# Optimization experiments

Hardware: AMD Instinct MI355X
Metric: run time of the kernel (lower is better)

Reference implementation:

```python
import jax, jax.numpy as jnp
import numpy as np

N, D, H, N_HEADS = 2048, 512, 512, 16

def setup_inputs() -> dict:
    key = jax.random.key(0)
    k1, k2, k3 = jax.random.split(key, 3)
    inputs = jax.random.normal(k1, (N, D), dtype=jnp.float32)
    idx = jax.random.randint(k2, (N,), 0, N_HEADS, dtype=jnp.int64)
    weights = jax.random.normal(k3, (N_HEADS, D, H), dtype=jnp.float32)
    biases = jnp.zeros((N_HEADS, H), dtype=jnp.float32)
    return {"inputs": inputs, "idx": idx, "weights": weights, "biases": biases}

def reference(inputs, idx, weights, biases):
    # per-sample weight gather: (N, D, H) then batched vec-mat: (N, 1, D) @ (N, D, H) -> (N, H)
    w = weights[idx]            # (N, D, H)  -- the redundant materialized gather
    b = biases[idx]             # (N, H)
    return jnp.einsum('nd,ndh->nh', inputs, w) + b
```

## Files before the change

### kernel.cpp

```cpp
#include <hip/hip_runtime.h>


#define N_SAMPLES 2048
#define DIM       512
#define HDIM      512
#define N_HEADS   16
#define SH        32
#define BPITCH    520

typedef __attribute__((ext_vector_type(8))) short bf16x8;
typedef __attribute__((ext_vector_type(4))) float floatx4;

__device__ inline unsigned short f2bf_rne(float f) {
    union { float f; unsigned u; } v; v.f = f;
    return (unsigned short)((v.u + 0x7FFFu + ((v.u >> 16) & 1u)) >> 16);
}
__device__ inline unsigned bfpack_rne(float lo, float hi) {
    return (unsigned)f2bf_rne(lo) | ((unsigned)f2bf_rne(hi) << 16);
}

__global__ __launch_bounds__(512, 2) void fused(
    const float* __restrict__ x,
    const int*   __restrict__ idx,
    const float* __restrict__ w,
    const float* __restrict__ bias,
    float*       __restrict__ out)
{
    __shared__ unsigned short Bl[SH * BPITCH];
    __shared__ unsigned short slist[N_SAMPLES];
    __shared__ int wcnt[8];

    const int bid  = blockIdx.x;
    const int head = 2 * (bid & 7) + ((bid >> 3) & 1);
    const int h0   = (bid >> 4) * SH;
    const int t    = threadIdx.x;
    const int wave = t >> 6;
    const int lane = t & 63;
    const int l16  = lane & 15;
    const int quad = lane >> 4;

    int myidx[4];
    #pragma unroll
    for (int c = 0; c < 4; ++c)
        myidx[c] = idx[(wave * 4 + c) * 64 + lane];

    const int hh = (t & 7) * 4;
    const int dg = t >> 3;
    const float* wg = w + (size_t)head * DIM * HDIM + h0;
    float4 q[8];
    #pragma unroll
    for (int s = 0; s < 8; ++s)
        q[s] = *(const float4*)(wg + (size_t)(dg * 8 + s) * HDIM + hh);

    unsigned long long masks[4];
    {
        int mycnt = 0;
        #pragma unroll
        for (int c = 0; c < 4; ++c) {
            masks[c] = __ballot(myidx[c] == head);
            mycnt += __popcll(masks[c]);
        }
        if (lane == 0) wcnt[wave] = mycnt;
    }
    __syncthreads();
    int cnt = 0, base = 0;
    #pragma unroll
    for (int i = 0; i < 8; ++i) { if (i < wave) base += wcnt[i]; cnt += wcnt[i]; }
    {
        int pos = base;
        #pragma unroll
        for (int c = 0; c < 4; ++c) {
            const unsigned long long m = masks[c];
            if (m & (1ull << lane)) {
                const int rank = __popcll(m & ((1ull << lane) - 1ull));
                slist[pos + rank] = (unsigned short)((wave * 4 + c) * 64 + lane);
            }
            pos += __popcll(m);
        }
    }

    #pragma unroll
    for (int k = 0; k < 4; ++k) {
        uint4 o;
        o.x = bfpack_rne(((const float*)&q[0])[k], ((const float*)&q[1])[k]);
        o.y = bfpack_rne(((const float*)&q[2])[k], ((const float*)&q[3])[k]);
        o.z = bfpack_rne(((const float*)&q[4])[k], ((const float*)&q[5])[k]);
        o.w = bfpack_rne(((const float*)&q[6])[k], ((const float*)&q[7])[k]);
        *(uint4*)&Bl[(hh + k) * BPITCH + dg * 8] = o;
    }
    __syncthreads();

    const int   mt  = (cnt + 15) >> 4;
    const float bv0 = bias[head * HDIM + h0 + l16];
    const float bv1 = bias[head * HDIM + h0 + 16 + l16];

    for (int j = wave; j < mt; j += 8) {
        const int mg  = j * 16 + l16;
        const int row = slist[mg < cnt ? mg : cnt - 1];
        const float* ap = x + (size_t)row * DIM + quad * 8;

        floatx4 acc0 = {0.f, 0.f, 0.f, 0.f};
        floatx4 acc1 = {0.f, 0.f, 0.f, 0.f};
        #pragma unroll
        for (int ks = 0; ks < 16; ++ks) {
            const float4 v0 = *(const float4*)(ap + ks * 32);
            const float4 v1 = *(const float4*)(ap + ks * 32 + 4);
            union { bf16x8 v; unsigned u[4]; } A;
            A.u[0] = bfpack_rne(v0.x, v0.y);
            A.u[1] = bfpack_rne(v0.z, v0.w);
            A.u[2] = bfpack_rne(v1.x, v1.y);
            A.u[3] = bfpack_rne(v1.z, v1.w);
            const bf16x8 b0 = *(const bf16x8*)&Bl[l16 * BPITCH + ks * 32 + quad * 8];
            const bf16x8 b1 = *(const bf16x8*)&Bl[(16 + l16) * BPITCH + ks * 32 + quad * 8];
            acc0 = __builtin_amdgcn_mfma_f32_16x16x32_bf16(A.v, b0, acc0, 0, 0, 0);
            acc1 = __builtin_amdgcn_mfma_f32_16x16x32_bf16(A.v, b1, acc1, 0, 0, 0);
        }

        #pragma unroll
        for (int r = 0; r < 4; ++r) {
            const int mm = j * 16 + quad * 4 + r;
            if (mm < cnt) {
                const int rg = slist[mm];
                out[(size_t)rg * HDIM + h0 + l16]      = acc0[r] + bv0;
                out[(size_t)rg * HDIM + h0 + 16 + l16] = acc1[r] + bv1;
            }
        }
    }
}

extern "C" void kernel_launch(void* const* d_in, const int* in_sizes, int n_in,
                              void* d_out, int out_size, void* d_ws, size_t ws_size,
                              hipStream_t stream) {
    const float* x   = (const float*)d_in[0];
    const int*   idx = (const int*)  d_in[1];
    const float* w   = (const float*)d_in[2];
    const float* b   = (const float*)d_in[3];
    float*       out = (float*)d_out;
    (void)d_ws; (void)ws_size;

    fused<<<N_HEADS * (HDIM / SH), 512, 0, stream>>>(x, idx, w, b, out);
}
```

Before: 87.05 us.

## Prefetch activation rows before weight staging; remap block-to-head order; nontemporal I/O

Adds a barrier after the sample list is built so each wave can issue global loads of its first 16 activation rows into registers while the weight tile is still being converted and written to LDS. This hides x-load latency behind the B-tile staging. It also changes the block-to-head mapping so consecutive blocks share a head, hoists the bias loads, and uses nontemporal loads for weights and nontemporal stores for outputs. Holding 32 float4 registers per thread raises register pressure at 512 threads with two blocks per CU, and the extra barrier adds a synchronisation.

```diff
diff --git a/kernel.cpp b/kernel.cpp
--- a/kernel.cpp
+++ b/kernel.cpp
@@ -31,8 +31,8 @@
     __shared__ int wcnt[8];
 
     const int bid  = blockIdx.x;
-    const int head = 2 * (bid & 7) + ((bid >> 3) & 1);
-    const int h0   = (bid >> 4) * SH;
+    const int head = bid >> 4;
+    const int h0   = (bid & 15) * SH;
     const int t    = threadIdx.x;
     const int wave = t >> 6;
     const int lane = t & 63;
@@ -44,13 +44,17 @@
     for (int c = 0; c < 4; ++c)
         myidx[c] = idx[(wave * 4 + c) * 64 + lane];
 
+    const float bv0 = bias[head * HDIM + h0 + l16];
+    const float bv1 = bias[head * HDIM + h0 + 16 + l16];
+
     const int hh = (t & 7) * 4;
     const int dg = t >> 3;
     const float* wg = w + (size_t)head * DIM * HDIM + h0;
-    float4 q[8];
+    floatx4 q[8];
     #pragma unroll
     for (int s = 0; s < 8; ++s)
-        q[s] = *(const float4*)(wg + (size_t)(dg * 8 + s) * HDIM + hh);
+        q[s] = __builtin_nontemporal_load(
+                   (const floatx4*)(wg + (size_t)(dg * 8 + s) * HDIM + hh));
 
     unsigned long long masks[4];
     {
@@ -78,6 +82,20 @@
             pos += __popcll(m);
         }
     }
+    __syncthreads();
+
+    const int mt = (cnt + 15) >> 4;
+    floatx4 xr[32];
+    if (wave < mt) {
+        const int mg  = wave * 16 + l16;
+        const int row = slist[mg < cnt ? mg : cnt - 1];
+        const float* ap = x + (size_t)row * DIM + quad * 8;
+        #pragma unroll
+        for (int ks = 0; ks < 16; ++ks) {
+            xr[2 * ks]     = *(const floatx4*)(ap + ks * 32);
+            xr[2 * ks + 1] = *(const floatx4*)(ap + ks * 32 + 4);
+        }
+    }
 
     #pragma unroll
     for (int k = 0; k < 4; ++k) {
@@ -90,21 +108,24 @@
     }
     __syncthreads();
 
-    const int   mt  = (cnt + 15) >> 4;
-    const float bv0 = bias[head * HDIM + h0 + l16];
-    const float bv1 = bias[head * HDIM + h0 + 16 + l16];
-
     for (int j = wave; j < mt; j += 8) {
-        const int mg  = j * 16 + l16;
-        const int row = slist[mg < cnt ? mg : cnt - 1];
-        const float* ap = x + (size_t)row * DIM + quad * 8;
+        if (j != wave) {
+            const int mg  = j * 16 + l16;
+            const int row = slist[mg < cnt ? mg : cnt - 1];
+            const float* ap = x + (size_t)row * DIM + quad * 8;
+            #pragma unroll
+            for (int ks = 0; ks < 16; ++ks) {
+                xr[2 * ks]     = *(const floatx4*)(ap + ks * 32);
+                xr[2 * ks + 1] = *(const floatx4*)(ap + ks * 32 + 4);
+            }
+        }
 
         floatx4 acc0 = {0.f, 0.f, 0.f, 0.f};
         floatx4 acc1 = {0.f, 0.f, 0.f, 0.f};
         #pragma unroll
         for (int ks = 0; ks < 16; ++ks) {
-            const float4 v0 = *(const float4*)(ap + ks * 32);
-            const float4 v1 = *(const float4*)(ap + ks * 32 + 4);
+            const floatx4 v0 = xr[2 * ks];
+            const floatx4 v1 = xr[2 * ks + 1];
             union { bf16x8 v; unsigned u[4]; } A;
             A.u[0] = bfpack_rne(v0.x, v0.y);
             A.u[1] = bfpack_rne(v0.z, v0.w);
@@ -121,8 +142,10 @@
             const int mm = j * 16 + quad * 4 + r;
             if (mm < cnt) {
                 const int rg = slist[mm];
-                out[(size_t)rg * HDIM + h0 + l16]      = acc0[r] + bv0;
-                out[(size_t)rg * HDIM + h0 + 16 + l16] = acc1[r] + bv1;
+                __builtin_nontemporal_store(acc0[r] + bv0,
+                    out + (size_t)rg * HDIM + h0 + l16);
+                __builtin_nontemporal_store(acc1[r] + bv1,
+                    out + (size_t)rg * HDIM + h0 + 16 + l16);
             }
         }
     }
```

Measured after the change: 85.25 us. 2.1% less time.
